# Kernel tuning notes

Hardware: AMD Instinct MI355X
Metric: run time of the kernel (lower is better)

## Reference

```python
import jax, jax.numpy as jnp
import numpy as np

N = 100000      # n_nodes
E = 1600000     # n_edges (avg degree 16)
D_IN, D_H, D_OUT = 128, 64, 16


def setup_inputs() -> dict:
    key = jax.random.key(0)
    k1, k2, k3, k4 = jax.random.split(key, 4)
    x = jax.random.normal(k1, (N, D_IN), dtype=jnp.float32)
    edge_index = jax.random.randint(k2, (2, E), 0, N, dtype=jnp.int32)
    W1 = jax.random.normal(k3, (D_IN, D_H), dtype=jnp.float32) / np.sqrt(D_IN)
    b1 = jnp.zeros((D_H,), dtype=jnp.float32)
    W2 = jax.random.normal(k4, (D_H, D_OUT), dtype=jnp.float32) / np.sqrt(D_H)
    b2 = jnp.zeros((D_OUT,), dtype=jnp.float32)
    return {"x": x, "edge_index": edge_index, "W1": W1, "b1": b1, "W2": W2, "b2": b2}


def gcn_conv(x, src, dst, W, b, n):
    """PyG GCNConv: linear transform, then deg^-1/2 A deg^-1/2 aggregation, + bias.
    src/dst already include self-loops."""
    h = x @ W                                              # [n, d_out]
    deg = jax.ops.segment_sum(jnp.ones_like(dst, dtype=h.dtype), dst, num_segments=n)
    dinv = jnp.where(deg > 0, jax.lax.rsqrt(jnp.maximum(deg, 1.0)), 0.0)
    norm = dinv[src] * dinv[dst]                           # [E+n]
    msgs = h[src] * norm[:, None]                          # gather + scale
    out = jax.ops.segment_sum(msgs, dst, num_segments=n)   # scatter-add
    return out + b


def reference(x, edge_index, W1, b1, W2, b2):
    loops = jnp.arange(N, dtype=edge_index.dtype)
    src = jnp.concatenate([edge_index[0], loops])
    dst = jnp.concatenate([edge_index[1], loops])
    h = jax.nn.relu(gcn_conv(x, src, dst, W1, b1, N))
    return gcn_conv(h, src, dst, W2, b2, N)
```

## Files before the change

kernel.cpp:

```cpp
#include <hip/hip_runtime.h>
#include <cstdint>

#define N_NODES 100000
#define N_EDGES 1600000
#define D_IN    128
#define D_H     64
#define D_OUT   16
#define M_TILES 6250

#define NBKT   512
#define NPB    196
#define BCAP   4096
#define TILE_E 4096
#define NTILES ((N_EDGES + TILE_E - 1) / TILE_E)
#define G1     128

typedef __attribute__((ext_vector_type(8))) short short8;
typedef __attribute__((ext_vector_type(4))) float floatx4;

static __device__ __forceinline__ unsigned short f2bf(float f) {
    unsigned int u = __float_as_uint(f);
    u = u + 0x7FFFu + ((u >> 16) & 1u);
    return (unsigned short)(u >> 16);
}
static __device__ __forceinline__ float bf2f(unsigned short h) {
    return __uint_as_float(((unsigned int)h) << 16);
}


__global__ __launch_bounds__(512) void zero_small_kernel(int* __restrict__ cursors,
                                                         int* __restrict__ srcs) {
    cursors[threadIdx.x] = 0;
    if (threadIdx.x < 16) srcs[N_EDGES + threadIdx.x] = 0;
}

__global__ __launch_bounds__(256) void bin_kernel(const int* __restrict__ src,
                                                  const int* __restrict__ dst,
                                                  int* __restrict__ cursors,
                                                  int* __restrict__ region) {
    __shared__ int hcnt[NBKT];
    __shared__ int hbase[NBKT];
    const int t = threadIdx.x;
    for (int tile = blockIdx.x; tile < NTILES; tile += gridDim.x) {
        for (int i = t; i < NBKT; i += 256) hcnt[i] = 0;
        __syncthreads();
        int e0 = tile * TILE_E + t * 16;
        int pk[16], bk[16], rk[16];
        bool full = (e0 + 16 <= N_EDGES);
        if (full) {
            const int4* dp = (const int4*)(dst + e0);
            const int4* sp = (const int4*)(src + e0);
            int dv[16], sv[16];
            #pragma unroll
            for (int q = 0; q < 4; ++q) {
                int4 d4 = dp[q]; int4 s4 = sp[q];
                dv[4*q+0]=d4.x; dv[4*q+1]=d4.y; dv[4*q+2]=d4.z; dv[4*q+3]=d4.w;
                sv[4*q+0]=s4.x; sv[4*q+1]=s4.y; sv[4*q+2]=s4.z; sv[4*q+3]=s4.w;
            }
            #pragma unroll
            for (int k = 0; k < 16; ++k) {
                int d = dv[k];
                int b = d / NPB;
                bk[k] = b;
                pk[k] = ((d - b * NPB) << 17) | sv[k];
                rk[k] = atomicAdd(&hcnt[b], 1);
            }
        }
        __syncthreads();
        for (int i = t; i < NBKT; i += 256) {
            int c = hcnt[i];
            if (c > 0) hbase[i] = atomicAdd(&cursors[i], c);
        }
        __syncthreads();
        if (full) {
            #pragma unroll
            for (int k = 0; k < 16; ++k)
                region[bk[k] * BCAP + hbase[bk[k]] + rk[k]] = pk[k];
        }
        __syncthreads();
    }
}

__global__ __launch_bounds__(256) void build_kernel(const int* __restrict__ cursors,
                                                    const int* __restrict__ region,
                                                    int* __restrict__ offsets,
                                                    float* __restrict__ dinv,
                                                    int* __restrict__ srcs) {
    __shared__ int lhist[NPB];
    __shared__ int lscan[NPB + 1];
    __shared__ int sbuf[256];
    __shared__ int srt[BCAP];
    __shared__ int red[4];
    int b = blockIdx.x;
    int t = threadIdx.x;

    int c0 = cursors[t];
    int c1 = cursors[t + 256];
    int p = ((t < b) ? c0 : 0) + ((t + 256 < b) ? c1 : 0);
    int lane = t & 63, wid = t >> 6;
    #pragma unroll
    for (int off = 32; off > 0; off >>= 1) p += __shfl_down(p, off);
    if (lane == 0) red[wid] = p;
    __syncthreads();
    int base = red[0] + red[1] + red[2] + red[3];
    int cnt = cursors[b];
    const int* reg = region + b * BCAP;

    for (int i = t; i < NPB; i += 256) lhist[i] = 0;
    __syncthreads();
    for (int i = t; i < cnt; i += 256) {
        int ln = reg[i] >> 17;
        atomicAdd(&lhist[ln], 1);
    }
    __syncthreads();
    int v = (t < NPB) ? lhist[t] : 0;
    sbuf[t] = v;
    __syncthreads();
    for (int off = 1; off < 256; off <<= 1) {
        int u = (t >= off) ? sbuf[t - off] : 0;
        __syncthreads();
        sbuf[t] += u;
        __syncthreads();
    }
    int incl = sbuf[t];
    if (t < NPB) lscan[t] = incl - v;
    if (t == NPB - 1) lscan[NPB] = incl;
    __syncthreads();
    if (t < NPB) lhist[t] = incl - v;
    __syncthreads();

    int node0 = b * NPB;
    int nlim = N_NODES - node0;
    if (nlim > NPB) nlim = NPB;
    if (t < nlim) {
        offsets[node0 + t] = base + lscan[t];
        int c = lscan[t + 1] - lscan[t];
        dinv[node0 + t] = rsqrtf((float)c + 1.0f);
    }
    if (b == (N_NODES - 1) / NPB && t == 0) offsets[N_NODES] = base + cnt;

    for (int i = t; i < cnt; i += 256) {
        int pk = reg[i];
        int ln = pk >> 17;
        int pos = atomicAdd(&lhist[ln], 1);
        srt[pos] = pk & 0x1FFFF;
    }
    __syncthreads();
    for (int i = t; i < cnt; i += 256) srcs[base + i] = srt[i];
}

__global__ __launch_bounds__(256) void gemm1_mfma_kernel(const float* __restrict__ x,
                                                         const float* __restrict__ W1,
                                                         const float* __restrict__ dinv,
                                                         unsigned short* __restrict__ hs) {
    __shared__ unsigned short bhi_lds[8192];
    __shared__ unsigned short blo_lds[8192];

    for (int e = threadIdx.x; e < 8192; e += 256) {
        int j    = e & 7;
        int lane = (e >> 3) & 63;
        int pair = e >> 9;
        int kc   = pair >> 2;
        int nt   = pair & 3;
        int k = kc * 32 + (lane >> 4) * 8 + j;
        int n = nt * 16 + (lane & 15);
        float w = W1[k * D_H + n];
        unsigned short hi = f2bf(w);
        float lo = w - bf2f(hi);
        bhi_lds[e] = hi;
        blo_lds[e] = f2bf(lo);
    }
    __syncthreads();

    int wid  = threadIdx.x >> 6;
    int lane = threadIdx.x & 63;
    int quad = lane >> 4;
    int m    = lane & 15;

    int tile = blockIdx.x * 4 + wid;
    if (tile >= M_TILES) return;
    int mbase = tile * 16;

    const float* xr = x + (size_t)(mbase + m) * D_IN + quad * 8;
    short8 ahi[4], alo[4];
    #pragma unroll
    for (int kc = 0; kc < 4; ++kc) {
        floatx4 v0 = *(const floatx4*)(xr + kc * 32);
        floatx4 v1 = *(const floatx4*)(xr + kc * 32 + 4);
        float f[8] = {v0.x, v0.y, v0.z, v0.w, v1.x, v1.y, v1.z, v1.w};
        #pragma unroll
        for (int j = 0; j < 8; ++j) {
            unsigned short hi = f2bf(f[j]);
            float lo = f[j] - bf2f(hi);
            ahi[kc][j] = (short)hi;
            alo[kc][j] = (short)f2bf(lo);
        }
    }

    floatx4 acc[4] = {{0.f,0.f,0.f,0.f},{0.f,0.f,0.f,0.f},{0.f,0.f,0.f,0.f},{0.f,0.f,0.f,0.f}};
    #pragma unroll
    for (int kc = 0; kc < 4; ++kc) {
        #pragma unroll
        for (int nt = 0; nt < 4; ++nt) {
            int fo = ((kc * 4 + nt) * 64 + lane) * 8;
            short8 bhi = *(const short8*)&bhi_lds[fo];
            short8 blo = *(const short8*)&blo_lds[fo];
            acc[nt] = __builtin_amdgcn_mfma_f32_16x16x32_bf16(ahi[kc], bhi, acc[nt], 0, 0, 0);
            acc[nt] = __builtin_amdgcn_mfma_f32_16x16x32_bf16(ahi[kc], blo, acc[nt], 0, 0, 0);
            acc[nt] = __builtin_amdgcn_mfma_f32_16x16x32_bf16(alo[kc], bhi, acc[nt], 0, 0, 0);
        }
    }

    float dv[4];
    #pragma unroll
    for (int r = 0; r < 4; ++r) dv[r] = dinv[mbase + quad * 4 + r];
    #pragma unroll
    for (int nt = 0; nt < 4; ++nt) {
        int col = nt * 16 + m;
        #pragma unroll
        for (int r = 0; r < 4; ++r) {
            int row = mbase + quad * 4 + r;
            hs[row * D_H + col] = f2bf(acc[nt][r] * dv[r]);
        }
    }
}

__global__ __launch_bounds__(256) void agg1_fused_kernel(const unsigned short* __restrict__ hs,
                                                         const int* __restrict__ offsets,
                                                         const int* __restrict__ srcs,
                                                         const float* __restrict__ dinv,
                                                         const float* __restrict__ b1,
                                                         const float* __restrict__ W2,
                                                         float* __restrict__ h2s) {
    __shared__ float rbuf[256];
    int wid  = threadIdx.x >> 6;
    int lane = threadIdx.x & 63;
    int wave = (blockIdx.x * blockDim.x + threadIdx.x) >> 6;
    int nwaves = (gridDim.x * blockDim.x) >> 6;

    int q = lane >> 4;
    int c = lane & 15;
    float w2c[16];
    #pragma unroll
    for (int j = 0; j < 16; ++j) w2c[j] = W2[(q * 16 + j) * D_OUT + c];
    float bias = b1[lane];
    float* myr = &rbuf[wid * 64];

    for (int node = wave; node < N_NODES; node += nwaves) {
        int beg = __builtin_amdgcn_readfirstlane(offsets[node]);
        int end = __builtin_amdgcn_readfirstlane(offsets[node + 1]);
        float acc = bf2f(hs[node * D_H + lane]);
        for (int e = beg; e < end; e += 16) {
            int rem = end - e;
            const int* ep = srcs + e;
            int jj[16];
            #pragma unroll
            for (int k = 0; k < 16; ++k)
                jj[k] = __builtin_amdgcn_readfirstlane(ep[k]);
            float vv[16];
            #pragma unroll
            for (int k = 0; k < 16; ++k) {
                const unsigned short* hp = hs + (size_t)jj[k] * D_H;
                vv[k] = bf2f(hp[lane]);
            }
            #pragma unroll
            for (int k = 0; k < 16; ++k) {
                float m = (k < rem) ? 1.0f : 0.0f;
                acc = fmaf(vv[k], m, acc);
            }
        }
        float dv = dinv[node];
        float r = fmaxf(acc * dv + bias, 0.f);

        myr[lane] = r;
        float part = 0.f;
        #pragma unroll
        for (int j = 0; j < 16; ++j) part += myr[q * 16 + j] * w2c[j];
        part += __shfl_xor(part, 16);
        part += __shfl_xor(part, 32);
        if (lane < 16) h2s[node * D_OUT + lane] = part * dv;
    }
}

__global__ __launch_bounds__(256) void agg2_kernel(const float* __restrict__ h2s,
                                                   const int* __restrict__ offsets,
                                                   const int* __restrict__ srcs,
                                                   const float* __restrict__ dinv,
                                                   const float* __restrict__ b2,
                                                   float* __restrict__ out) {
    int col = threadIdx.x & 15;
    int nidx = (blockIdx.x * blockDim.x + threadIdx.x) >> 4;
    int stride = (gridDim.x * blockDim.x) >> 4;
    for (int node = nidx; node < N_NODES; node += stride) {
        int beg = offsets[node], end = offsets[node + 1];
        float acc = h2s[node * D_OUT + col];
        for (int e = beg; e < end; e += 16) {
            int rem = end - e;
            const int* ep = srcs + e;
            int jj[16];
            #pragma unroll
            for (int k = 0; k < 16; ++k) jj[k] = ep[k];
            float vv[16];
            #pragma unroll
            for (int k = 0; k < 16; ++k) vv[k] = h2s[jj[k] * D_OUT + col];
            #pragma unroll
            for (int k = 0; k < 16; ++k) {
                float m = (k < rem) ? 1.0f : 0.0f;
                acc = fmaf(vv[k], m, acc);
            }
        }
        out[node * D_OUT + col] = acc * dinv[node] + b2[col];
    }
}

extern "C" void kernel_launch(void* const* d_in, const int* in_sizes, int n_in,
                              void* d_out, int out_size, void* d_ws, size_t ws_size,
                              hipStream_t stream) {
    const float* x  = (const float*)d_in[0];
    const int*   ei = (const int*)d_in[1];
    const float* W1 = (const float*)d_in[2];
    const float* b1 = (const float*)d_in[3];
    const float* W2 = (const float*)d_in[4];
    const float* b2 = (const float*)d_in[5];
    float* out = (float*)d_out;

    const int* src = ei;
    const int* dst = ei + N_EDGES;

    char* w = (char*)d_ws;
    int*   cursors  = (int*)(w + 0);
    int*   offsets  = (int*)(w + 4096);
    float* dinv     = (float*)(w + 404224);
    int*   srcs     = (int*)(w + 804224);
    unsigned short* hs = (unsigned short*)(w + 7204352);
    float* h2s      = (float*)(w + 20004480);
    int*   region   = (int*)(w + 26404480);

    zero_small_kernel<<<1, 512, 0, stream>>>(cursors, srcs);
    bin_kernel<<<G1, 256, 0, stream>>>(src, dst, cursors, region);
    build_kernel<<<NBKT, 256, 0, stream>>>(cursors, region, offsets, dinv, srcs);
    gemm1_mfma_kernel<<<(M_TILES + 3) / 4, 256, 0, stream>>>(x, W1, dinv, hs);
    agg1_fused_kernel<<<6250, 256, 0, stream>>>(hs, offsets, srcs, dinv, b1, W2, h2s);
    agg2_kernel<<<6250, 256, 0, stream>>>(h2s, offsets, srcs, dinv, b2, out);
}
```

Baseline: 204.4 us.

## Restructure layer-1 aggregation to 16 threads per node with vectorized gathers

```diff
diff --git a/kernel.cpp b/kernel.cpp
--- a/kernel.cpp
+++ b/kernel.cpp
@@ -13,7 +13,7 @@
 #define BCAP   4096
 #define TILE_E 4096
 #define NTILES ((N_EDGES + TILE_E - 1) / TILE_E)
-#define G1     128
+#define G1     256
 
 typedef __attribute__((ext_vector_type(8))) short short8;
 typedef __attribute__((ext_vector_type(4))) float floatx4;
@@ -232,54 +232,58 @@
                                                          const float* __restrict__ b1,
                                                          const float* __restrict__ W2,
                                                          float* __restrict__ h2s) {
-    __shared__ float rbuf[256];
-    int wid  = threadIdx.x >> 6;
-    int lane = threadIdx.x & 63;
-    int wave = (blockIdx.x * blockDim.x + threadIdx.x) >> 6;
-    int nwaves = (gridDim.x * blockDim.x) >> 6;
-
-    int q = lane >> 4;
-    int c = lane & 15;
-    float w2c[16];
-    #pragma unroll
-    for (int j = 0; j < 16; ++j) w2c[j] = W2[(q * 16 + j) * D_OUT + c];
-    float bias = b1[lane];
-    float* myr = &rbuf[wid * 64];
-
-    for (int node = wave; node < N_NODES; node += nwaves) {
-        int beg = __builtin_amdgcn_readfirstlane(offsets[node]);
-        int end = __builtin_amdgcn_readfirstlane(offsets[node + 1]);
-        float acc = bf2f(hs[node * D_H + lane]);
-        for (int e = beg; e < end; e += 16) {
-            int rem = end - e;
-            const int* ep = srcs + e;
-            int jj[16];
-            #pragma unroll
-            for (int k = 0; k < 16; ++k)
-                jj[k] = __builtin_amdgcn_readfirstlane(ep[k]);
-            float vv[16];
-            #pragma unroll
-            for (int k = 0; k < 16; ++k) {
-                const unsigned short* hp = hs + (size_t)jj[k] * D_H;
-                vv[k] = bf2f(hp[lane]);
-            }
-            #pragma unroll
-            for (int k = 0; k < 16; ++k) {
-                float m = (k < rem) ? 1.0f : 0.0f;
-                acc = fmaf(vv[k], m, acc);
-            }
-        }
-        float dv = dinv[node];
-        float r = fmaxf(acc * dv + bias, 0.f);
-
-        myr[lane] = r;
-        float part = 0.f;
+    __shared__ float w2t[16 * 68];
+    __shared__ float rbuf[16 * 68];
+
+    const int tid = threadIdx.x;
+    for (int i = tid; i < 1024; i += 256) {
+        int j = i >> 4, c = i & 15;
+        w2t[c * 68 + j] = W2[i];
+    }
+
+    const int g    = tid >> 4;
+    const int sl   = tid & 15;
+    const int node = blockIdx.x * 16 + g;
+    const int c4   = sl * 4;
+
+    const int beg = offsets[node];
+    const int end = offsets[node + 1];
+
+    ushort4 s4v = *(const ushort4*)(hs + (size_t)node * D_H + c4);
+    float a0 = bf2f(s4v.x), a1 = bf2f(s4v.y), a2 = bf2f(s4v.z), a3 = bf2f(s4v.w);
+
+    for (int e = beg; e < end; e += 16) {
+        int rem = end - e;
+        int idx = srcs[e + sl];
         #pragma unroll
-        for (int j = 0; j < 16; ++j) part += myr[q * 16 + j] * w2c[j];
-        part += __shfl_xor(part, 16);
-        part += __shfl_xor(part, 32);
-        if (lane < 16) h2s[node * D_OUT + lane] = part * dv;
-    }
+        for (int k = 0; k < 16; ++k) {
+            int j = __shfl(idx, k, 16);
+            ushort4 v = *(const ushort4*)(hs + (size_t)j * D_H + c4);
+            float m = (k < rem) ? 1.0f : 0.0f;
+            a0 = fmaf(bf2f(v.x), m, a0);
+            a1 = fmaf(bf2f(v.y), m, a1);
+            a2 = fmaf(bf2f(v.z), m, a2);
+            a3 = fmaf(bf2f(v.w), m, a3);
+        }
+    }
+
+    const float dv = dinv[node];
+    const floatx4 bb = *(const floatx4*)(b1 + c4);
+    float* rb = rbuf + g * 68;
+    rb[c4 + 0] = fmaxf(a0 * dv + bb.x, 0.f);
+    rb[c4 + 1] = fmaxf(a1 * dv + bb.y, 0.f);
+    rb[c4 + 2] = fmaxf(a2 * dv + bb.z, 0.f);
+    rb[c4 + 3] = fmaxf(a3 * dv + bb.w, 0.f);
+    __syncthreads();
+
+    float p = 0.f;
+    #pragma unroll
+    for (int t4 = 0; t4 < 16; ++t4) {
+        floatx4 rv = *(const floatx4*)(rb + 4 * t4);
+        floatx4 wv = *(const floatx4*)(&w2t[sl * 68 + 4 * t4]);
+        p += rv.x * wv.x + rv.y * wv.y + rv.z * wv.z + rv.w * wv.w;
+    }
+    h2s[node * D_OUT + sl] = p * dv;
 }
 
 __global__ __launch_bounds__(256) void agg2_kernel(const float* __restrict__ h2s,
```

Result: no change. 200.9 us (-1.7%).
